# Performance work log

Hardware: AMD Instinct MI355X
Metric: run time of the kernel (lower is better)

Reference implementation:

```python
import jax, jax.numpy as jnp
import numpy as np

N_USERS = 50000
N_ITEMS = 50000
N_NODES = N_USERS + N_ITEMS
N_EDGES = 1600000
N_PAIRS = 200000
USER_DIM = 128
ITEM_DIM = 128
HID = 64
LAYER_NUM = 2


def setup_inputs() -> dict:
    key = jax.random.key(0)
    ks = jax.random.split(key, 16)
    inp = {
        "user_features": jax.random.normal(ks[0], (N_USERS, USER_DIM), jnp.float32),
        "item_features": jax.random.normal(ks[1], (N_ITEMS, ITEM_DIM), jnp.float32),
        "item_side_feat": jax.random.normal(ks[2], (N_ITEMS, HID), jnp.float32),
        "T_f": jax.random.uniform(ks[3], (2 * N_PAIRS,), jnp.float32),
        "T_cf": jax.random.uniform(ks[4], (2 * N_PAIRS,), jnp.float32),
        "Wu": jax.random.normal(ks[5], (USER_DIM, HID), jnp.float32) / np.sqrt(USER_DIM),
        "bu": jax.random.normal(ks[6], (HID,), jnp.float32) * 0.01,
        "Wi": jax.random.normal(ks[7], (ITEM_DIM, HID), jnp.float32) / np.sqrt(ITEM_DIM),
        "bi": jax.random.normal(ks[8], (HID,), jnp.float32) * 0.01,
        "W1": jax.random.normal(ks[9], (1 + 2 * HID, HID), jnp.float32) / np.sqrt(1 + 2 * HID),
        "b1": jax.random.normal(ks[10], (HID,), jnp.float32) * 0.01,
        "W2": jax.random.normal(ks[11], (HID, 1), jnp.float32) / np.sqrt(HID),
        "edge_src": jax.random.randint(ks[12], (N_EDGES,), 0, N_NODES, jnp.int32),
        "edge_dst": jax.random.randint(ks[13], (N_EDGES,), 0, N_NODES, jnp.int32),
        "userId": jax.random.randint(ks[14], (N_PAIRS,), 0, N_USERS, jnp.int32),
        "pos_itemId": jax.random.randint(ks[15], (N_PAIRS,), 0, N_ITEMS, jnp.int32),
        "neg_itemId": jax.random.randint(jax.random.fold_in(key, 99), (N_PAIRS,), 0, N_ITEMS, jnp.int32),
    }
    return inp


def reference(user_features, item_features, item_side_feat, T_f, T_cf,
              Wu, bu, Wi, bi, W1, b1, W2,
              edge_src, edge_dst, userId, pos_itemId, neg_itemId):
    # degree-based symmetric normalization (out_deg^-0.5 on src, in_deg^-0.5 on dst)
    ones = jnp.ones((edge_src.shape[0],), jnp.float32)
    out_deg = jax.ops.segment_sum(ones, edge_src, num_segments=N_NODES)
    in_deg = jax.ops.segment_sum(ones, edge_dst, num_segments=N_NODES)
    out_norm = jax.lax.rsqrt(jnp.clip(out_deg, 1.0))[:, None]  # [N,1]
    in_norm = jax.lax.rsqrt(jnp.clip(in_deg, 1.0))[:, None]

    def gcn_layer(node_f):
        m = node_f * out_norm                                   # [N,H]
        agg = jax.ops.segment_sum(m[edge_src], edge_dst, num_segments=N_NODES)
        return agg * in_norm

    user_embedding = jax.nn.relu(user_features @ Wu + bu)       # [Nu,H]
    item_embedding = jax.nn.relu(item_features @ Wi + bi)       # [Ni,H]

    for i in range(LAYER_NUM):
        if i == 0:
            embeddings = gcn_layer(jnp.concatenate([user_embedding, item_embedding], axis=0))
        else:
            embeddings = gcn_layer(embeddings)
        scale = 1.0 / (i + 2)
        user_embedding = user_embedding + embeddings[:N_USERS] * scale
        item_embedding = item_embedding + embeddings[N_USERS:] * scale

    item_embedding = item_embedding + item_side_feat

    userE = user_embedding[userId]                              # [P,H]
    posE = item_embedding[pos_itemId]
    negE = item_embedding[neg_itemId]
    zi = jnp.concatenate([userE, userE], axis=0)                # [2P,H]
    zj = jnp.concatenate([posE, negE], axis=0)

    def decode(T):
        h = jnp.concatenate([zi, zj, T[:, None]], axis=1)       # [2P, 2H+1]
        h = jax.nn.elu(h @ W1 + b1)
        return (h @ W2)[:, 0]                                   # [2P]

    logits_f = decode(T_f)
    logits_cf = decode(T_cf)
    return (user_embedding, item_embedding, logits_f, logits_cf)
```

## Files before the change

### kernel.cpp

```cpp
#include <hip/hip_runtime.h>

#define NU 50000
#define NI 50000
#define NN 100000
#define NE 1600000
#define NP 200000
#define DIM 128
#define HID 64

#define HR 4
#define HC 32
#define RN (NN / HR)
#define RNW (RN / 2)
#define CE (NE / HC)

typedef unsigned short bf16_t;
typedef __attribute__((ext_vector_type(8))) short short8;
typedef __attribute__((ext_vector_type(4))) float f32x4;
typedef __attribute__((ext_vector_type(2))) float f32x2;

__device__ __forceinline__ float bf2f(unsigned short u) {
  union { unsigned int i; float f; } c; c.i = ((unsigned int)u) << 16; return c.f;
}
__device__ __forceinline__ unsigned short f2bf(float f) {
  union { float f; unsigned int i; } c; c.f = f;
  unsigned int i = c.i;
  i += 0x7fffu + ((i >> 16) & 1u);
  return (unsigned short)(i >> 16);
}
__device__ __forceinline__ f32x2 unpack2(unsigned int w) {
  union { unsigned int i; float f; } lo, hi;
  lo.i = w << 16;
  hi.i = w & 0xffff0000u;
  f32x2 r; r.x = lo.f; r.y = hi.f;
  return r;
}
__device__ __forceinline__ int geti(const void* p, int i, bool i64) {
  return i64 ? (int)((const long long*)p)[i] : ((const int*)p)[i];
}

__global__ __launch_bounds__(64) void k_detect(const bf16_t* __restrict__ uf,
                                               const int* __restrict__ ei,
                                               int* __restrict__ flag) {
  int lane = threadIdx.x;
  float m = 0.f;
  for (int i = lane; i < 4096; i += 64) {
    float v = fabsf(bf2f(uf[i]));
    if (v < 3e38f) m = fmaxf(m, v);
  }
  int cnt = 0;
  for (int i = lane; i < 4096; i += 64) {
    if (ei[2 * i + 1] == 0) cnt++;
  }
  for (int off = 32; off > 0; off >>= 1) {
    m = fmaxf(m, __shfl_xor(m, off));
    cnt += __shfl_xor(cnt, off);
  }
  if (lane == 0) {
    flag[0] = (m > 100.f) ? 1 : 0;
    flag[1] = (cnt > 2048) ? 1 : 0;
  }
}

__global__ __launch_bounds__(1024) void k_hist(const void* __restrict__ srcv,
                                               const void* __restrict__ dstv,
                                               const int* __restrict__ flag,
                                               int* __restrict__ pout,
                                               int* __restrict__ pin) {
  __shared__ unsigned int ho[RNW];
  __shared__ unsigned int hd[RNW];
  const bool i64 = (flag[1] != 0);
  int r = blockIdx.x & (HR - 1);
  int c = blockIdx.x >> 2;
  int lo = r * RN, hiN = lo + RN;
  int t = threadIdx.x;
  for (int i = t; i < RNW; i += 1024) { ho[i] = 0u; hd[i] = 0u; }
  __syncthreads();
  int ebeg = c * CE;
  if (!i64) {
    const int* sp = (const int*)srcv + ebeg;
    const int* dp = (const int*)dstv + ebeg;
    for (int e = t * 4; e < CE; e += 1024 * 4) {
      int4 sv = *(const int4*)(sp + e);
      int4 dv = *(const int4*)(dp + e);
      int ss[4] = {sv.x, sv.y, sv.z, sv.w};
      int dd[4] = {dv.x, dv.y, dv.z, dv.w};
#pragma unroll
      for (int k = 0; k < 4; ++k) {
        int s = ss[k];
        if (s >= lo && s < hiN) {
          int loc = s - lo;
          atomicAdd(&ho[loc >> 1], 1u << ((loc & 1) * 16));
        }
        int d = dd[k];
        if (d >= lo && d < hiN) {
          int loc = d - lo;
          atomicAdd(&hd[loc >> 1], 1u << ((loc & 1) * 16));
        }
      }
    }
  } else {
    const long long* sp = (const long long*)srcv + ebeg;
    const long long* dp = (const long long*)dstv + ebeg;
    for (int e = t; e < CE; e += 1024) {
      int s = (int)sp[e];
      if (s >= lo && s < hiN) {
        int loc = s - lo;
        atomicAdd(&ho[loc >> 1], 1u << ((loc & 1) * 16));
      }
      int d = (int)dp[e];
      if (d >= lo && d < hiN) {
        int loc = d - lo;
        atomicAdd(&hd[loc >> 1], 1u << ((loc & 1) * 16));
      }
    }
  }
  __syncthreads();
  int* po = pout + c * NN + lo;
  int* pi = pin + c * NN + lo;
  for (int i = t; i < RNW; i += 1024) {
    unsigned int o = ho[i], d = hd[i];
    int2 ov; ov.x = (int)(o & 0xffffu); ov.y = (int)(o >> 16);
    int2 dv; dv.x = (int)(d & 0xffffu); dv.y = (int)(d >> 16);
    *(int2*)(po + 2 * i) = ov;
    *(int2*)(pi + 2 * i) = dv;
  }
}

__global__ __launch_bounds__(256) void k_reduce(const int* __restrict__ pout,
                                                int* __restrict__ pin,
                                                int* __restrict__ din,
                                                float* __restrict__ onorm,
                                                float* __restrict__ inorm) {
  int n = blockIdx.x * 256 + threadIdx.x;
  if (n >= NN) return;
  int so = 0;
#pragma unroll
  for (int c = 0; c < HC; ++c) so += pout[c * NN + n];
  int si = 0;
#pragma unroll
  for (int c = 0; c < HC; ++c) {
    int v = pin[c * NN + n];
    pin[c * NN + n] = si;
    si += v;
  }
  din[n] = si;
  onorm[n] = rsqrtf((float)(so > 1 ? so : 1));
  inorm[n] = rsqrtf((float)(si > 1 ? si : 1));
}

__global__ __launch_bounds__(256) void k_scan1(const int* __restrict__ in,
                                               int* __restrict__ bsums, int n) {
  __shared__ int sh[256];
  int t = threadIdx.x;
  int base = blockIdx.x * 1024 + t * 4;
  int s = 0;
#pragma unroll
  for (int i = 0; i < 4; ++i)
    if (base + i < n) s += in[base + i];
  sh[t] = s;
  __syncthreads();
  for (int off = 128; off > 0; off >>= 1) {
    if (t < off) sh[t] += sh[t + off];
    __syncthreads();
  }
  if (t == 0) bsums[blockIdx.x] = sh[0];
}

__global__ __launch_bounds__(128) void k_scan2(const int* __restrict__ bsums,
                                               int* __restrict__ boffs, int nb) {
  __shared__ int sh[128];
  int t = threadIdx.x;
  int own = (t < nb) ? bsums[t] : 0;
  sh[t] = own;
  __syncthreads();
  for (int off = 1; off < 128; off <<= 1) {
    int add = (t >= off) ? sh[t - off] : 0;
    __syncthreads();
    sh[t] += add;
    __syncthreads();
  }
  if (t < nb) boffs[t] = sh[t] - own;
}

__global__ __launch_bounds__(256) void k_scan3(const int* __restrict__ in,
                                               const int* __restrict__ boffs,
                                               int* __restrict__ row_ptr, int n) {
  __shared__ int sh[256];
  int t = threadIdx.x;
  int base = blockIdx.x * 1024 + t * 4;
  int v[4];
  int s = 0;
#pragma unroll
  for (int i = 0; i < 4; ++i) {
    v[i] = (base + i < n) ? in[base + i] : 0;
    s += v[i];
  }
  sh[t] = s;
  __syncthreads();
  for (int off = 1; off < 256; off <<= 1) {
    int add = (t >= off) ? sh[t - off] : 0;
    __syncthreads();
    sh[t] += add;
    __syncthreads();
  }
  int excl = boffs[blockIdx.x] + sh[t] - s;
#pragma unroll
  for (int i = 0; i < 4; ++i) {
    if (base + i < n) {
      row_ptr[base + i] = excl;
      excl += v[i];
    }
  }
  if (blockIdx.x == 0 && t == 0) row_ptr[n] = NE;
}

__global__ __launch_bounds__(1024) void k_fill2(const void* __restrict__ srcv,
                                                const void* __restrict__ dstv,
                                                const int* __restrict__ flag,
                                                const int* __restrict__ row_ptr,
                                                const int* __restrict__ pin,
                                                int* __restrict__ csr_src) {
  __shared__ int cur[RN];
  const bool i64 = (flag[1] != 0);
  int r = blockIdx.x & (HR - 1);
  int c = blockIdx.x >> 2;
  int lo = r * RN, hiN = lo + RN;
  int t = threadIdx.x;
  const int* pi = pin + c * NN + lo;
  const int* rp = row_ptr + lo;
  for (int i = t; i < RN; i += 1024) cur[i] = rp[i] + pi[i];
  __syncthreads();
  int ebeg = c * CE;
  if (!i64) {
    const int* sp = (const int*)srcv + ebeg;
    const int* dp = (const int*)dstv + ebeg;
    for (int e = t * 4; e < CE; e += 1024 * 4) {
      int4 dv = *(const int4*)(dp + e);
      int4 sv = *(const int4*)(sp + e);
      int dd[4] = {dv.x, dv.y, dv.z, dv.w};
      int ss[4] = {sv.x, sv.y, sv.z, sv.w};
#pragma unroll
      for (int k = 0; k < 4; ++k) {
        int d = dd[k];
        if (d >= lo && d < hiN) {
          int slot = atomicAdd(&cur[d - lo], 1);
          csr_src[slot] = ss[k];
        }
      }
    }
  } else {
    const long long* sp = (const long long*)srcv + ebeg;
    const long long* dp = (const long long*)dstv + ebeg;
    for (int e = t; e < CE; e += 1024) {
      int d = (int)dp[e];
      if (d >= lo && d < hiN) {
        int slot = atomicAdd(&cur[d - lo], 1);
        csr_src[slot] = (int)sp[e];
      }
    }
  }
}

__global__ __launch_bounds__(256) void k_embed(const void* __restrict__ featv,
                                               const void* __restrict__ Wv,
                                               const void* __restrict__ biasv,
                                               const int* __restrict__ flag,
                                               const float* __restrict__ onorm_base,
                                               float* __restrict__ out,
                                               bf16_t* __restrict__ embs, int rows) {
  __shared__ float Ws[DIM * HID];
  __shared__ float bs[HID];
  const bool f32 = (flag[0] != 0);
  int t = threadIdx.x;
  if (f32) {
    const float* W = (const float*)Wv;
    for (int i = t; i < DIM * HID; i += 256) Ws[i] = W[i];
    if (t < HID) bs[t] = ((const float*)biasv)[t];
  } else {
    const bf16_t* W = (const bf16_t*)Wv;
    for (int i = t; i < DIM * HID; i += 256) Ws[i] = bf2f(W[i]);
    if (t < HID) bs[t] = bf2f(((const bf16_t*)biasv)[t]);
  }
  __syncthreads();
  int rl = t >> 4;
  int jq = t & 15;
  for (int rbase = blockIdx.x * 16; rbase < rows; rbase += gridDim.x * 16) {
    int row = rbase + rl;
    if (row >= rows) continue;
    float a0 = 0.f, a1 = 0.f, a2 = 0.f, a3 = 0.f;
    if (f32) {
      const float* fr = (const float*)featv + (size_t)row * DIM;
      for (int k0 = 0; k0 < DIM; k0 += 4) {
        float4 f4 = *(const float4*)(fr + k0);
        float fk[4] = {f4.x, f4.y, f4.z, f4.w};
#pragma unroll
        for (int kk = 0; kk < 4; ++kk) {
          const float* wr = &Ws[(k0 + kk) * HID + jq * 4];
          a0 += fk[kk] * wr[0];
          a1 += fk[kk] * wr[1];
          a2 += fk[kk] * wr[2];
          a3 += fk[kk] * wr[3];
        }
      }
    } else {
      const bf16_t* fr = (const bf16_t*)featv + (size_t)row * DIM;
      for (int k0 = 0; k0 < DIM; k0 += 8) {
        uint4 u = *(const uint4*)(fr + k0);
        unsigned int w[4] = {u.x, u.y, u.z, u.w};
#pragma unroll
        for (int kk = 0; kk < 8; ++kk) {
          unsigned short us = (unsigned short)((w[kk >> 1] >> ((kk & 1) * 16)) & 0xffffu);
          float fk = bf2f(us);
          const float* wr = &Ws[(k0 + kk) * HID + jq * 4];
          a0 += fk * wr[0];
          a1 += fk * wr[1];
          a2 += fk * wr[2];
          a3 += fk * wr[3];
        }
      }
    }
    float4 r;
    r.x = fmaxf(a0 + bs[jq * 4 + 0], 0.f);
    r.y = fmaxf(a1 + bs[jq * 4 + 1], 0.f);
    r.z = fmaxf(a2 + bs[jq * 4 + 2], 0.f);
    r.w = fmaxf(a3 + bs[jq * 4 + 3], 0.f);
    *(float4*)&out[(size_t)row * HID + jq * 4] = r;
    float sc = onorm_base[row];
    uint2 p;
    p.x = (unsigned int)f2bf(r.x * sc) | ((unsigned int)f2bf(r.y * sc) << 16);
    p.y = (unsigned int)f2bf(r.z * sc) | ((unsigned int)f2bf(r.w * sc) << 16);
    *(uint2*)&embs[(size_t)row * HID + jq * 4] = p;
  }
}

__global__ __launch_bounds__(256) void k_gather1(const bf16_t* __restrict__ embs,
                                                 const float* __restrict__ onorm,
                                                 const float* __restrict__ inorm,
                                                 const int* __restrict__ row_ptr,
                                                 const int* __restrict__ csr_src,
                                                 bf16_t* __restrict__ e1s) {
  int n = blockIdx.x * 4 + (threadIdx.x >> 6);
  if (n >= NN) return;
  int lane = threadIdx.x & 63;
  int g = lane >> 3;
  int l8 = (lane & 7) * 8;
  int beg = row_ptr[n], end = row_ptr[n + 1];
  f32x2 a[4];
#pragma unroll
  for (int j = 0; j < 4; ++j) a[j] = (f32x2)(0.f);
  for (int base = beg; base < end; base += 32) {
    int ev[4], sv[4];
#pragma unroll
    for (int k = 0; k < 4; ++k) {
      int ee = base + k * 8 + g;
      ev[k] = ee;
      sv[k] = csr_src[ee < end ? ee : end - 1];
    }
#pragma unroll
    for (int k = 0; k < 4; ++k) {
      uint4 u = *(const uint4*)(embs + (size_t)sv[k] * HID + l8);
      unsigned int msk = (ev[k] < end) ? 0xffffffffu : 0u;
      a[0] += unpack2(u.x & msk);
      a[1] += unpack2(u.y & msk);
      a[2] += unpack2(u.z & msk);
      a[3] += unpack2(u.w & msk);
    }
  }
#pragma unroll
  for (int j = 0; j < 4; ++j) {
    a[j].x += __shfl_xor(a[j].x, 8);
    a[j].y += __shfl_xor(a[j].y, 8);
    a[j].x += __shfl_xor(a[j].x, 16);
    a[j].y += __shfl_xor(a[j].y, 16);
    a[j].x += __shfl_xor(a[j].x, 32);
    a[j].y += __shfl_xor(a[j].y, 32);
  }
  if (g == 0) {
    float sc = inorm[n] * onorm[n];
    uint4 p;
    p.x = (unsigned int)f2bf(a[0].x * sc) | ((unsigned int)f2bf(a[0].y * sc) << 16);
    p.y = (unsigned int)f2bf(a[1].x * sc) | ((unsigned int)f2bf(a[1].y * sc) << 16);
    p.z = (unsigned int)f2bf(a[2].x * sc) | ((unsigned int)f2bf(a[2].y * sc) << 16);
    p.w = (unsigned int)f2bf(a[3].x * sc) | ((unsigned int)f2bf(a[3].y * sc) << 16);
    *(uint4*)(e1s + (size_t)n * HID + l8) = p;
  }
}

__global__ __launch_bounds__(256) void k_gather2c(float* __restrict__ emb0,
                                                  const bf16_t* __restrict__ e1s,
                                                  const void* __restrict__ sidev,
                                                  const int* __restrict__ flag,
                                                  const float* __restrict__ onorm,
                                                  const float* __restrict__ inorm,
                                                  const int* __restrict__ row_ptr,
                                                  const int* __restrict__ csr_src,
                                                  bf16_t* __restrict__ fin_bf) {
  int n = blockIdx.x * 4 + (threadIdx.x >> 6);
  if (n >= NN) return;
  int lane = threadIdx.x & 63;
  int g = lane >> 3;
  int l8 = (lane & 7) * 8;
  int beg = row_ptr[n], end = row_ptr[n + 1];
  f32x2 a[4];
#pragma unroll
  for (int j = 0; j < 4; ++j) a[j] = (f32x2)(0.f);
  for (int base = beg; base < end; base += 32) {
    int ev[4], sv[4];
#pragma unroll
    for (int k = 0; k < 4; ++k) {
      int ee = base + k * 8 + g;
      ev[k] = ee;
      sv[k] = csr_src[ee < end ? ee : end - 1];
    }
#pragma unroll
    for (int k = 0; k < 4; ++k) {
      uint4 u = *(const uint4*)(e1s + (size_t)sv[k] * HID + l8);
      unsigned int msk = (ev[k] < end) ? 0xffffffffu : 0u;
      a[0] += unpack2(u.x & msk);
      a[1] += unpack2(u.y & msk);
      a[2] += unpack2(u.z & msk);
      a[3] += unpack2(u.w & msk);
    }
  }
#pragma unroll
  for (int j = 0; j < 4; ++j) {
    a[j].x += __shfl_xor(a[j].x, 8);
    a[j].y += __shfl_xor(a[j].y, 8);
    a[j].x += __shfl_xor(a[j].x, 16);
    a[j].y += __shfl_xor(a[j].y, 16);
    a[j].x += __shfl_xor(a[j].x, 32);
    a[j].y += __shfl_xor(a[j].y, 32);
  }
  if (g == 0) {
    float aa[8] = {a[0].x, a[0].y, a[1].x, a[1].y, a[2].x, a[2].y, a[3].x, a[3].y};
    float inorm_n = inorm[n];
    float inv_on = 1.0f / onorm[n];
    size_t off = (size_t)n * HID + l8;
    uint4 u = *(const uint4*)(e1s + off);
    unsigned int w[4] = {u.x, u.y, u.z, u.w};
    float e1v[8];
#pragma unroll
    for (int j = 0; j < 4; ++j) {
      e1v[2 * j]     = bf2f((unsigned short)(w[j] & 0xffffu)) * inv_on;
      e1v[2 * j + 1] = bf2f((unsigned short)(w[j] >> 16)) * inv_on;
    }
    float4 b0 = *(const float4*)&emb0[off];
    float4 b1 = *(const float4*)&emb0[off + 4];
    float bb[8] = {b0.x, b0.y, b0.z, b0.w, b1.x, b1.y, b1.z, b1.w};
    const float s2 = 1.f / 3.f;
    float vv[8];
#pragma unroll
    for (int j = 0; j < 8; ++j)
      vv[j] = bb[j] + 0.5f * e1v[j] + s2 * aa[j] * inorm_n;
    if (n >= NU) {
      size_t soff = (size_t)(n - NU) * HID + l8;
      if (flag[0] != 0) {
        float4 s0 = *(const float4*)((const float*)sidev + soff);
        float4 s1 = *(const float4*)((const float*)sidev + soff + 4);
        vv[0] += s0.x; vv[1] += s0.y; vv[2] += s0.z; vv[3] += s0.w;
        vv[4] += s1.x; vv[5] += s1.y; vv[6] += s1.z; vv[7] += s1.w;
      } else {
        uint4 su = *(const uint4*)((const bf16_t*)sidev + soff);
        unsigned int sw[4] = {su.x, su.y, su.z, su.w};
#pragma unroll
        for (int j = 0; j < 4; ++j) {
          vv[2 * j]     += bf2f((unsigned short)(sw[j] & 0xffffu));
          vv[2 * j + 1] += bf2f((unsigned short)(sw[j] >> 16));
        }
      }
    }
    float4 o0, o1;
    o0.x = vv[0]; o0.y = vv[1]; o0.z = vv[2]; o0.w = vv[3];
    o1.x = vv[4]; o1.y = vv[5]; o1.z = vv[6]; o1.w = vv[7];
    *(float4*)&emb0[off] = o0;
    *(float4*)&emb0[off + 4] = o1;
    uint4 pb;
    pb.x = (unsigned int)f2bf(vv[0]) | ((unsigned int)f2bf(vv[1]) << 16);
    pb.y = (unsigned int)f2bf(vv[2]) | ((unsigned int)f2bf(vv[3]) << 16);
    pb.z = (unsigned int)f2bf(vv[4]) | ((unsigned int)f2bf(vv[5]) << 16);
    pb.w = (unsigned int)f2bf(vv[6]) | ((unsigned int)f2bf(vv[7]) << 16);
    *(uint4*)(fin_bf + off) = pb;
  }
}

__global__ __launch_bounds__(256) void k_decode(const bf16_t* __restrict__ zb,
                                                const void* __restrict__ W1v,
                                                const void* __restrict__ b1v,
                                                const void* __restrict__ W2v,
                                                const void* __restrict__ Tfv,
                                                const void* __restrict__ Tcfv,
                                                const int* __restrict__ flag,
                                                const void* __restrict__ userId,
                                                const void* __restrict__ posId,
                                                const void* __restrict__ negId,
                                                float* __restrict__ out_lf,
                                                float* __restrict__ out_lcf) {
  __shared__ bf16_t W1b[128 * 65];
  __shared__ float wlast[HID], b1s[HID], W2s[HID];
  const bool f32 = (flag[0] != 0);
  const bool i64 = (flag[1] != 0);
  int t = threadIdx.x;
  if (f32) {
    const float* W1 = (const float*)W1v;
    for (int i = t; i < 128 * 64; i += 256) W1b[(i >> 6) * 65 + (i & 63)] = f2bf(W1[i]);
    if (t < HID) {
      wlast[t] = W1[128 * 64 + t];
      b1s[t] = ((const float*)b1v)[t];
      W2s[t] = ((const float*)W2v)[t];
    }
  } else {
    const bf16_t* W1 = (const bf16_t*)W1v;
    for (int i = t; i < 128 * 64; i += 256) W1b[(i >> 6) * 65 + (i & 63)] = W1[i];
    if (t < HID) {
      wlast[t] = bf2f(W1[128 * 64 + t]);
      b1s[t] = bf2f(((const bf16_t*)b1v)[t]);
      W2s[t] = bf2f(((const bf16_t*)W2v)[t]);
    }
  }
  __syncthreads();
  int wv = t >> 6;
  int lane = t & 63;
  int m = lane & 15;
  int q = lane >> 4;
  short8 Bf[4][4];
#pragma unroll
  for (int c = 0; c < 4; ++c)
#pragma unroll
    for (int nt = 0; nt < 4; ++nt)
#pragma unroll
      for (int j = 0; j < 8; ++j)
        Bf[c][nt][j] = (short)W1b[(c * 32 + q * 8 + j) * 65 + nt * 16 + m];

  const int tiles = NP / 16;
  for (int tile = blockIdx.x * 4 + wv; tile < tiles; tile += gridDim.x * 4) {
    int pid = tile * 16 + m;
    int uid = geti(userId, pid, i64);
    int pidx = geti(posId, pid, i64);
    int nidx = geti(negId, pid, i64);
    const bf16_t* ur = zb + (size_t)uid * HID;
    const bf16_t* pp = zb + (size_t)(NU + pidx) * HID;
    const bf16_t* nn = zb + (size_t)(NU + nidx) * HID;
    short8 au0 = *(const short8*)(ur + q * 8);
    short8 au1 = *(const short8*)(ur + 32 + q * 8);
    short8 ap0 = *(const short8*)(pp + q * 8);
    short8 ap1 = *(const short8*)(pp + 32 + q * 8);
    short8 an0 = *(const short8*)(nn + q * 8);
    short8 an1 = *(const short8*)(nn + 32 + q * 8);
    f32x4 accp[4], accn[4];
#pragma unroll
    for (int nt = 0; nt < 4; ++nt) {
      f32x4 accu = (f32x4)(0.f);
      accu = __builtin_amdgcn_mfma_f32_16x16x32_bf16(au0, Bf[0][nt], accu, 0, 0, 0);
      accu = __builtin_amdgcn_mfma_f32_16x16x32_bf16(au1, Bf[1][nt], accu, 0, 0, 0);
      accp[nt] = __builtin_amdgcn_mfma_f32_16x16x32_bf16(ap0, Bf[2][nt], accu, 0, 0, 0);
      accp[nt] = __builtin_amdgcn_mfma_f32_16x16x32_bf16(ap1, Bf[3][nt], accp[nt], 0, 0, 0);
      accn[nt] = __builtin_amdgcn_mfma_f32_16x16x32_bf16(an0, Bf[2][nt], accu, 0, 0, 0);
      accn[nt] = __builtin_amdgcn_mfma_f32_16x16x32_bf16(an1, Bf[3][nt], accn[nt], 0, 0, 0);
    }
    float tf_p[4], tc_p[4], tf_n[4], tc_n[4];
    int rbase = tile * 16 + q * 4;
    if (f32) {
      float4 t4 = *(const float4*)((const float*)Tfv + rbase);
      float4 c4 = *(const float4*)((const float*)Tcfv + rbase);
      float4 t4n = *(const float4*)((const float*)Tfv + rbase + NP);
      float4 c4n = *(const float4*)((const float*)Tcfv + rbase + NP);
      tf_p[0] = t4.x; tf_p[1] = t4.y; tf_p[2] = t4.z; tf_p[3] = t4.w;
      tc_p[0] = c4.x; tc_p[1] = c4.y; tc_p[2] = c4.z; tc_p[3] = c4.w;
      tf_n[0] = t4n.x; tf_n[1] = t4n.y; tf_n[2] = t4n.z; tf_n[3] = t4n.w;
      tc_n[0] = c4n.x; tc_n[1] = c4n.y; tc_n[2] = c4n.z; tc_n[3] = c4n.w;
    } else {
      const bf16_t* tp = (const bf16_t*)Tfv + rbase;
      const bf16_t* cp = (const bf16_t*)Tcfv + rbase;
#pragma unroll
      for (int r = 0; r < 4; ++r) {
        tf_p[r] = bf2f(tp[r]); tc_p[r] = bf2f(cp[r]);
        tf_n[r] = bf2f(tp[r + NP]); tc_n[r] = bf2f(cp[r + NP]);
      }
    }
#pragma unroll
    for (int r = 0; r < 4; ++r) {
      float sfp = 0.f, scp = 0.f, sfn = 0.f, scn = 0.f;
#pragma unroll
      for (int nt = 0; nt < 4; ++nt) {
        int n = nt * 16 + m;
        float b = b1s[n];
        float wl = wlast[n];
        float w2 = W2s[n];
        float xp = accp[nt][r] + b;
        float xn = accn[nt][r] + b;
        float v0 = xp + tf_p[r] * wl;
        float v1 = xp + tc_p[r] * wl;
        float v2 = xn + tf_n[r] * wl;
        float v3 = xn + tc_n[r] * wl;
        sfp += (v0 > 0.f ? v0 : (__expf(v0) - 1.f)) * w2;
        scp += (v1 > 0.f ? v1 : (__expf(v1) - 1.f)) * w2;
        sfn += (v2 > 0.f ? v2 : (__expf(v2) - 1.f)) * w2;
        scn += (v3 > 0.f ? v3 : (__expf(v3) - 1.f)) * w2;
      }
#pragma unroll
      for (int s = 1; s < 16; s <<= 1) {
        sfp += __shfl_xor(sfp, s);
        scp += __shfl_xor(scp, s);
        sfn += __shfl_xor(sfn, s);
        scn += __shfl_xor(scn, s);
      }
      if (m == 0) {
        int pr2 = rbase + r;
        out_lf[pr2] = sfp;
        out_lcf[pr2] = scp;
        out_lf[pr2 + NP] = sfn;
        out_lcf[pr2 + NP] = scn;
      }
    }
  }
}

extern "C" void kernel_launch(void* const* d_in, const int* in_sizes, int n_in,
                              void* d_out, int out_size, void* d_ws, size_t ws_size,
                              hipStream_t stream) {
  (void)in_sizes; (void)n_in; (void)out_size;
  const void* user_f = d_in[0];
  const void* item_f = d_in[1];
  const void* side   = d_in[2];
  const void* Tf     = d_in[3];
  const void* Tcf    = d_in[4];
  const void* Wu     = d_in[5];
  const void* bu     = d_in[6];
  const void* Wi     = d_in[7];
  const void* bi     = d_in[8];
  const void* W1     = d_in[9];
  const void* b1     = d_in[10];
  const void* W2     = d_in[11];
  const void* esrc   = d_in[12];
  const void* edst   = d_in[13];
  const void* userId = d_in[14];
  const void* posId  = d_in[15];
  const void* negId  = d_in[16];

  const size_t WS_NEEDED = 33601280;
  if (ws_size < WS_NEEDED) return;

  char* ws = (char*)d_ws;
  int*   deg_in  = (int*)(ws + 0);
  float* onorm   = (float*)(ws + 400000);
  float* inorm   = (float*)(ws + 800000);
  int*   row_ptr = (int*)(ws + 1200000);
  int*   bsums   = (int*)(ws + 1600128);
  int*   boffs   = (int*)(ws + 1600640);
  int*   flag    = (int*)(ws + 1601152);
  int*   csr_src = (int*)(ws + 1601280);
  int*   pout    = (int*)(ws + 8001280);
  int*   pin     = (int*)(ws + 20801280);
  bf16_t* embs   = (bf16_t*)(ws + 8001280);
  bf16_t* e1s    = (bf16_t*)(ws + 20801280);
  bf16_t* fin_bf = embs;

  float* out     = (float*)d_out;
  float* emb0    = out;
  float* out_lf  = out + (size_t)NN * HID;
  float* out_lcf = out_lf + 2 * NP;

  k_detect<<<1, 64, 0, stream>>>((const bf16_t*)user_f, (const int*)esrc, flag);
  k_hist<<<HR * HC, 1024, 0, stream>>>(esrc, edst, flag, pout, pin);
  k_reduce<<<(NN + 255) / 256, 256, 0, stream>>>(pout, pin, deg_in, onorm, inorm);
  k_scan1<<<98, 256, 0, stream>>>(deg_in, bsums, NN);
  k_scan2<<<1, 128, 0, stream>>>(bsums, boffs, 98);
  k_scan3<<<98, 256, 0, stream>>>(deg_in, boffs, row_ptr, NN);
  k_fill2<<<HR * HC, 1024, 0, stream>>>(esrc, edst, flag, row_ptr, pin, csr_src);
  k_embed<<<256, 256, 0, stream>>>(user_f, Wu, bu, flag, onorm, emb0, embs, NU);
  k_embed<<<256, 256, 0, stream>>>(item_f, Wi, bi, flag, onorm + NU,
                                   emb0 + (size_t)NU * HID, embs + (size_t)NU * HID, NI);
  k_gather1<<<NN / 4, 256, 0, stream>>>(embs, onorm, inorm, row_ptr, csr_src, e1s);
  k_gather2c<<<NN / 4, 256, 0, stream>>>(emb0, e1s, side, flag, onorm, inorm, row_ptr,
                                         csr_src, fin_bf);
  k_decode<<<1024, 256, 0, stream>>>(fin_bf, W1, b1, W2, Tf, Tcf, flag,
                                     userId, posId, negId, out_lf, out_lcf);
}
```

Baseline: 427.1 us.

## Split degree histograms per direction, pack counts as u16 pairs, pad gathers with zero row

The combined src/dst histogram kernel becomes two launches of a single-array histogram. Each uses 2 node ranges and 64 edge chunks, and partials are stored as packed 16-bit pairs, which halves partial traffic in the reduce and fill stages. The CSR gather loops drop the per-edge masking by pointing out-of-range lanes at a zero sentinel row (index NN) and padding csr_src with sentinel entries. This trades an extra launch and more blocks for less shared-memory pressure and fewer ALU ops. It also relies on 16-bit per-chunk counts not overflowing.

Measured after the change: 419.6 us. About the same (-1.8%).

```diff
diff --git a/kernel.cpp b/kernel.cpp
--- a/kernel.cpp
+++ b/kernel.cpp
@@ -8,11 +8,14 @@
 #define DIM 128
 #define HID 64
 
-#define HR 4
-#define HC 32
-#define RN (NN / HR)
-#define RNW (RN / 2)
-#define CE (NE / HC)
+#define HR2 2
+#define HC2 64
+#define RN2 (NN / HR2)
+#define RNW2 (RN2 / 2)
+#define CE2 (NE / HC2)
+
+#define HRF 4
+#define RNF (NN / HRF)
 
 typedef unsigned short bf16_t;
 typedef __attribute__((ext_vector_type(8))) short short8;
@@ -62,91 +65,76 @@
   }
 }
 
-__global__ __launch_bounds__(1024) void k_hist(const void* __restrict__ srcv,
-                                               const void* __restrict__ dstv,
-                                               const int* __restrict__ flag,
-                                               int* __restrict__ pout,
-                                               int* __restrict__ pin) {
-  __shared__ unsigned int ho[RNW];
-  __shared__ unsigned int hd[RNW];
+__global__ __launch_bounds__(1024) void k_hist1(const void* __restrict__ ev,
+                                                const int* __restrict__ flag,
+                                                unsigned int* __restrict__ part) {
+  __shared__ unsigned int h[RNW2];
   const bool i64 = (flag[1] != 0);
-  int r = blockIdx.x & (HR - 1);
-  int c = blockIdx.x >> 2;
-  int lo = r * RN, hiN = lo + RN;
+  int r = blockIdx.x & (HR2 - 1);
+  int c = blockIdx.x >> 1;
+  int lo = r * RN2, hiN = lo + RN2;
   int t = threadIdx.x;
-  for (int i = t; i < RNW; i += 1024) { ho[i] = 0u; hd[i] = 0u; }
-  __syncthreads();
-  int ebeg = c * CE;
+  for (int i = t; i < RNW2; i += 1024) h[i] = 0u;
+  __syncthreads();
+  int ebeg = c * CE2;
   if (!i64) {
-    const int* sp = (const int*)srcv + ebeg;
-    const int* dp = (const int*)dstv + ebeg;
-    for (int e = t * 4; e < CE; e += 1024 * 4) {
-      int4 sv = *(const int4*)(sp + e);
-      int4 dv = *(const int4*)(dp + e);
-      int ss[4] = {sv.x, sv.y, sv.z, sv.w};
-      int dd[4] = {dv.x, dv.y, dv.z, dv.w};
+    const int* p = (const int*)ev + ebeg;
+    for (int e = t * 4; e < CE2; e += 1024 * 4) {
+      int4 v4 = *(const int4*)(p + e);
+      int vv[4] = {v4.x, v4.y, v4.z, v4.w};
 #pragma unroll
       for (int k = 0; k < 4; ++k) {
-        int s = ss[k];
-        if (s >= lo && s < hiN) {
-          int loc = s - lo;
-          atomicAdd(&ho[loc >> 1], 1u << ((loc & 1) * 16));
+        int v = vv[k];
+        if (v >= lo && v < hiN) {
+          int loc = v - lo;
+          atomicAdd(&h[loc >> 1], 1u << ((loc & 1) * 16));
         }
-        int d = dd[k];
-        if (d >= lo && d < hiN) {
-          int loc = d - lo;
-          atomicAdd(&hd[loc >> 1], 1u << ((loc & 1) * 16));
-        }
       }
     }
   } else {
-    const long long* sp = (const long long*)srcv + ebeg;
-    const long long* dp = (const long long*)dstv + ebeg;
-    for (int e = t; e < CE; e += 1024) {
-      int s = (int)sp[e];
-      if (s >= lo && s < hiN) {
-        int loc = s - lo;
-        atomicAdd(&ho[loc >> 1], 1u << ((loc & 1) * 16));
-      }
-      int d = (int)dp[e];
-      if (d >= lo && d < hiN) {
-        int loc = d - lo;
-        atomicAdd(&hd[loc >> 1], 1u << ((loc & 1) * 16));
-      }
-    }
-  }
-  __syncthreads();
-  int* po = pout + c * NN + lo;
-  int* pi = pin + c * NN + lo;
-  for (int i = t; i < RNW; i += 1024) {
-    unsigned int o = ho[i], d = hd[i];
-    int2 ov; ov.x = (int)(o & 0xffffu); ov.y = (int)(o >> 16);
-    int2 dv; dv.x = (int)(d & 0xffffu); dv.y = (int)(d >> 16);
-    *(int2*)(po + 2 * i) = ov;
-    *(int2*)(pi + 2 * i) = dv;
-  }
-}
-
-__global__ __launch_bounds__(256) void k_reduce(const int* __restrict__ pout,
-                                                int* __restrict__ pin,
+    const long long* p = (const long long*)ev + ebeg;
+    for (int e = t; e < CE2; e += 1024) {
+      int v = (int)p[e];
+      if (v >= lo && v < hiN) {
+        int loc = v - lo;
+        atomicAdd(&h[loc >> 1], 1u << ((loc & 1) * 16));
+      }
+    }
+  }
+  __syncthreads();
+  unsigned int* po = part + c * (NN / 2) + (lo >> 1);
+  for (int i = t; i < RNW2; i += 1024) po[i] = h[i];
+}
+
+__global__ __launch_bounds__(256) void k_reduce(const unsigned int* __restrict__ pout,
+                                                unsigned int* __restrict__ pin,
                                                 int* __restrict__ din,
                                                 float* __restrict__ onorm,
                                                 float* __restrict__ inorm) {
-  int n = blockIdx.x * 256 + threadIdx.x;
-  if (n >= NN) return;
-  int so = 0;
-#pragma unroll
-  for (int c = 0; c < HC; ++c) so += pout[c * NN + n];
-  int si = 0;
-#pragma unroll
-  for (int c = 0; c < HC; ++c) {
-    int v = pin[c * NN + n];
-    pin[c * NN + n] = si;
-    si += v;
-  }
-  din[n] = si;
-  onorm[n] = rsqrtf((float)(so > 1 ? so : 1));
-  inorm[n] = rsqrtf((float)(si > 1 ? si : 1));
+  int w = blockIdx.x * 256 + threadIdx.x;
+  if (w >= NN / 2) return;
+  unsigned int so0 = 0, so1 = 0;
+#pragma unroll
+  for (int c = 0; c < HC2; ++c) {
+    unsigned int v = pout[c * (NN / 2) + w];
+    so0 += v & 0xffffu;
+    so1 += v >> 16;
+  }
+  unsigned int si0 = 0, si1 = 0;
+#pragma unroll
+  for (int c = 0; c < HC2; ++c) {
+    unsigned int v = pin[c * (NN / 2) + w];
+    pin[c * (NN / 2) + w] = si0 | (si1 << 16);
+    si0 += v & 0xffffu;
+    si1 += v >> 16;
+  }
+  int n = 2 * w;
+  din[n] = (int)si0;
+  din[n + 1] = (int)si1;
+  onorm[n] = rsqrtf((float)(so0 > 1u ? so0 : 1u));
+  onorm[n + 1] = rsqrtf((float)(so1 > 1u ? so1 : 1u));
+  inorm[n] = rsqrtf((float)(si0 > 1u ? si0 : 1u));
+  inorm[n + 1] = rsqrtf((float)(si1 > 1u ? si1 : 1u));
 }
 
 __global__ __launch_bounds__(256) void k_scan1(const int* __restrict__ in,
@@ -185,7 +173,8 @@
 
 __global__ __launch_bounds__(256) void k_scan3(const int* __restrict__ in,
                                                const int* __restrict__ boffs,
-                                               int* __restrict__ row_ptr, int n) {
+                                               int* __restrict__ row_ptr,
+                                               int* __restrict__ csr_src, int n) {
   __shared__ int sh[256];
   int t = threadIdx.x;
   int base = blockIdx.x * 1024 + t * 4;
@@ -213,29 +202,35 @@
     }
   }
   if (blockIdx.x == 0 && t == 0) row_ptr[n] = NE;
+  if (blockIdx.x == 0 && t < 32) csr_src[NE + t] = NN;
 }
 
 __global__ __launch_bounds__(1024) void k_fill2(const void* __restrict__ srcv,
                                                 const void* __restrict__ dstv,
                                                 const int* __restrict__ flag,
                                                 const int* __restrict__ row_ptr,
-                                                const int* __restrict__ pin,
+                                                const unsigned int* __restrict__ pin,
                                                 int* __restrict__ csr_src) {
-  __shared__ int cur[RN];
+  __shared__ int cur[RNF];
   const bool i64 = (flag[1] != 0);
-  int r = blockIdx.x & (HR - 1);
+  int r = blockIdx.x & (HRF - 1);
   int c = blockIdx.x >> 2;
-  int lo = r * RN, hiN = lo + RN;
+  int lo = r * RNF, hiN = lo + RNF;
   int t = threadIdx.x;
-  const int* pi = pin + c * NN + lo;
+  const unsigned int* pw = pin + c * (NN / 2);
   const int* rp = row_ptr + lo;
-  for (int i = t; i < RN; i += 1024) cur[i] = rp[i] + pi[i];
-  __syncthreads();
-  int ebeg = c * CE;
+  for (int i = t; i < RNF; i += 1024) {
+    int node = lo + i;
+    unsigned int wrd = pw[node >> 1];
+    int off = (int)((wrd >> ((node & 1) * 16)) & 0xffffu);
+    cur[i] = rp[i] + off;
+  }
+  __syncthreads();
+  int ebeg = c * CE2;
   if (!i64) {
     const int* sp = (const int*)srcv + ebeg;
     const int* dp = (const int*)dstv + ebeg;
-    for (int e = t * 4; e < CE; e += 1024 * 4) {
+    for (int e = t * 4; e < CE2; e += 1024 * 4) {
       int4 dv = *(const int4*)(dp + e);
       int4 sv = *(const int4*)(sp + e);
       int dd[4] = {dv.x, dv.y, dv.z, dv.w};
@@ -252,7 +247,7 @@
   } else {
     const long long* sp = (const long long*)srcv + ebeg;
     const long long* dp = (const long long*)dstv + ebeg;
-    for (int e = t; e < CE; e += 1024) {
+    for (int e = t; e < CE2; e += 1024) {
       int d = (int)dp[e];
       if (d >= lo && d < hiN) {
         int slot = atomicAdd(&cur[d - lo], 1);
@@ -268,11 +263,14 @@
                                                const int* __restrict__ flag,
                                                const float* __restrict__ onorm_base,
                                                float* __restrict__ out,
-                                               bf16_t* __restrict__ embs, int rows) {
+                                               bf16_t* __restrict__ embs,
+                                               bf16_t* __restrict__ zrow, int rows) {
   __shared__ float Ws[DIM * HID];
   __shared__ float bs[HID];
   const bool f32 = (flag[0] != 0);
   int t = threadIdx.x;
+  if (zrow && blockIdx.x == 0 && t < 32)
+    ((unsigned int*)zrow)[t] = 0u;
   if (f32) {
     const float* W = (const float*)Wv;
     for (int i = t; i < DIM * HID; i += 256) Ws[i] = W[i];
@@ -340,6 +338,8 @@
                                                  const int* __restrict__ row_ptr,
                                                  const int* __restrict__ csr_src,
                                                  bf16_t* __restrict__ e1s) {
+  if (blockIdx.x == 0 && threadIdx.x < 32)
+    ((unsigned int*)(e1s + (size_t)NN * HID))[threadIdx.x] = 0u;
   int n = blockIdx.x * 4 + (threadIdx.x >> 6);
   if (n >= NN) return;
   int lane = threadIdx.x & 63;
@@ -350,21 +350,20 @@
 #pragma unroll
   for (int j = 0; j < 4; ++j) a[j] = (f32x2)(0.f);
   for (int base = beg; base < end; base += 32) {
-    int ev[4], sv[4];
+    int sv[4];
 #pragma unroll
     for (int k = 0; k < 4; ++k) {
       int ee = base + k * 8 + g;
-      ev[k] = ee;
-      sv[k] = csr_src[ee < end ? ee : end - 1];
+      int raw = csr_src[ee];
+      sv[k] = (ee < end) ? raw : NN;
     }
 #pragma unroll
     for (int k = 0; k < 4; ++k) {
-      uint4 u = *(const uint4*)(embs + (size_t)sv[k] * HID + l8);
-      unsigned int msk = (ev[k] < end) ? 0xffffffffu : 0u;
-      a[0] += unpack2(u.x & msk);
-      a[1] += unpack2(u.y & msk);
-      a[2] += unpack2(u.z & msk);
-      a[3] += unpack2(u.w & msk);
+      uint4 u = *(const uint4*)(embs + (sv[k] << 6) + l8);
+      a[0] += unpack2(u.x);
+      a[1] += unpack2(u.y);
+      a[2] += unpack2(u.z);
+      a[3] += unpack2(u.w);
     }
   }
 #pragma unroll
@@ -406,21 +405,20 @@
 #pragma unroll
   for (int j = 0; j < 4; ++j) a[j] = (f32x2)(0.f);
   for (int base = beg; base < end; base += 32) {
-    int ev[4], sv[4];
+    int sv[4];
 #pragma unroll
     for (int k = 0; k < 4; ++k) {
       int ee = base + k * 8 + g;
-      ev[k] = ee;
-      sv[k] = csr_src[ee < end ? ee : end - 1];
+      int raw = csr_src[ee];
+      sv[k] = (ee < end) ? raw : NN;
     }
 #pragma unroll
     for (int k = 0; k < 4; ++k) {
-      uint4 u = *(const uint4*)(e1s + (size_t)sv[k] * HID + l8);
-      unsigned int msk = (ev[k] < end) ? 0xffffffffu : 0u;
-      a[0] += unpack2(u.x & msk);
-      a[1] += unpack2(u.y & msk);
-      a[2] += unpack2(u.z & msk);
-      a[3] += unpack2(u.w & msk);
+      uint4 u = *(const uint4*)(e1s + (sv[k] << 6) + l8);
+      a[0] += unpack2(u.x);
+      a[1] += unpack2(u.y);
+      a[2] += unpack2(u.z);
+      a[3] += unpack2(u.w);
     }
   }
 #pragma unroll
@@ -638,7 +636,7 @@
   const void* posId  = d_in[15];
   const void* negId  = d_in[16];
 
-  const size_t WS_NEEDED = 33601280;
+  const size_t WS_NEEDED = 33601664;
   if (ws_size < WS_NEEDED) return;
 
   char* ws = (char*)d_ws;
@@ -650,10 +648,10 @@
   int*   boffs   = (int*)(ws + 1600640);
   int*   flag    = (int*)(ws + 1601152);
   int*   csr_src = (int*)(ws + 1601280);
-  int*   pout    = (int*)(ws + 8001280);
-  int*   pin     = (int*)(ws + 20801280);
-  bf16_t* embs   = (bf16_t*)(ws + 8001280);
-  bf16_t* e1s    = (bf16_t*)(ws + 20801280);
+  unsigned int* pout = (unsigned int*)(ws + 8001408);
+  unsigned int* pin  = (unsigned int*)(ws + 20801536);
+  bf16_t* embs   = (bf16_t*)(ws + 8001408);
+  bf16_t* e1s    = (bf16_t*)(ws + 20801536);
   bf16_t* fin_bf = embs;
 
   float* out     = (float*)d_out;
@@ -662,15 +660,18 @@
   float* out_lcf = out_lf + 2 * NP;
 
   k_detect<<<1, 64, 0, stream>>>((const bf16_t*)user_f, (const int*)esrc, flag);
-  k_hist<<<HR * HC, 1024, 0, stream>>>(esrc, edst, flag, pout, pin);
-  k_reduce<<<(NN + 255) / 256, 256, 0, stream>>>(pout, pin, deg_in, onorm, inorm);
+  k_hist1<<<HR2 * HC2, 1024, 0, stream>>>(esrc, flag, pout);
+  k_hist1<<<HR2 * HC2, 1024, 0, stream>>>(edst, flag, pin);
+  k_reduce<<<(NN / 2 + 255) / 256, 256, 0, stream>>>(pout, pin, deg_in, onorm, inorm);
   k_scan1<<<98, 256, 0, stream>>>(deg_in, bsums, NN);
   k_scan2<<<1, 128, 0, stream>>>(bsums, boffs, 98);
-  k_scan3<<<98, 256, 0, stream>>>(deg_in, boffs, row_ptr, NN);
-  k_fill2<<<HR * HC, 1024, 0, stream>>>(esrc, edst, flag, row_ptr, pin, csr_src);
-  k_embed<<<256, 256, 0, stream>>>(user_f, Wu, bu, flag, onorm, emb0, embs, NU);
+  k_scan3<<<98, 256, 0, stream>>>(deg_in, boffs, row_ptr, csr_src, NN);
+  k_fill2<<<HRF * HC2, 1024, 0, stream>>>(esrc, edst, flag, row_ptr, pin, csr_src);
+  k_embed<<<256, 256, 0, stream>>>(user_f, Wu, bu, flag, onorm, emb0, embs,
+                                   embs + (size_t)NN * HID, NU);
   k_embed<<<256, 256, 0, stream>>>(item_f, Wi, bi, flag, onorm + NU,
-                                   emb0 + (size_t)NU * HID, embs + (size_t)NU * HID, NI);
+                                   emb0 + (size_t)NU * HID, embs + (size_t)NU * HID,
+                                   (bf16_t*)0, NI);
   k_gather1<<<NN / 4, 256, 0, stream>>>(embs, onorm, inorm, row_ptr, csr_src, e1s);
   k_gather2c<<<NN / 4, 256, 0, stream>>>(emb0, e1s, side, flag, onorm, inorm, row_ptr,
                                          csr_src, fin_bf);
```
